# Kernel tuning notes

Hardware: AMD Instinct MI355X
Metric: run time of the kernel (lower is better)

Reference implementation:

```python
import jax, jax.numpy as jnp
import numpy as np

IN_F = 512
OUT_F = 512
ALPHA = 0.2   # LeakyReLU negative slope
NEG_INF = -9e15


def setup_inputs() -> dict:
    key = jax.random.key(0)
    k1, k2, k3, k4 = jax.random.split(key, 4)
    B, S = 8, 2048
    hidden_state = jax.random.normal(k1, (B, S, IN_F), dtype=jnp.float32)
    adjacent_matrix = jax.random.uniform(k2, (B, S, S), dtype=jnp.float32)
    # nn.Linear weight (no bias): stored as [out, in] in torch; we keep [in, out] for x @ W
    bound = 1.0 / np.sqrt(IN_F)
    W = jax.random.uniform(k3, (IN_F, OUT_F), dtype=jnp.float32, minval=-bound, maxval=bound)
    # xavier_uniform with gain=1.414 on a: shape [2*out, 1]
    a_bound = 1.414 * np.sqrt(6.0 / (2 * OUT_F + 1))
    a = jax.random.uniform(k4, (2 * OUT_F, 1), dtype=jnp.float32, minval=-a_bound, maxval=a_bound)
    return {"hidden_state": hidden_state, "adjacent_matrix": adjacent_matrix, "W": W, "a": a}


def reference(hidden_state, adjacent_matrix, W, a):
    # Wh: [B, S, out]
    Wh = jnp.einsum('bsi,io->bso', hidden_state, W)
    # additive attention: Wh1 + Wh2^T -> [B, S, S]
    Wh1 = Wh @ a[:OUT_F, :]            # [B, S, 1]
    Wh2 = Wh @ a[OUT_F:, :]            # [B, S, 1]
    e = Wh1 + jnp.swapaxes(Wh2, 1, 2)  # [B, S, S]
    e = jax.nn.leaky_relu(e, negative_slope=ALPHA)
    attention = jnp.where(adjacent_matrix > 0.5, e, NEG_INF)
    # NOTE: original softmaxes over dim=1 (the *row* index), faithfully reproduced
    attention = jax.nn.softmax(attention, axis=1)
    # dropout is identity at inference (training=False)
    h_prime = jnp.einsum('bst,bto->bso', attention, Wh)
    return jax.nn.elu(h_prime)  # concat=True path
```

## Files before the change

kernel.cpp:

```cpp
#include <hip/hip_runtime.h>
#include <hip/hip_bf16.h>
#include <stdint.h>

#define SDIM 2048
#define BDIM 8
#define FDIM 512
constexpr float ALPHA = 0.2f;

typedef __attribute__((ext_vector_type(8))) short bf16x8;
typedef __attribute__((ext_vector_type(4))) float f32x4;

__device__ __forceinline__ unsigned short f2bf(float x) {
  __hip_bfloat16 h = __float2bfloat16(x);
  return *reinterpret_cast<unsigned short*>(&h);
}

__device__ __forceinline__ void gload_lds16(const void* g, void* l) {
  __builtin_amdgcn_global_load_lds(
      (const __attribute__((address_space(1))) unsigned int*)(uintptr_t)g,
      (__attribute__((address_space(3))) unsigned int*)(uintptr_t)l,
      16, 0, 0);
}

__global__ void k0_prep(const float* __restrict__ W, const float* __restrict__ a,
                        float* __restrict__ wa, __hip_bfloat16* __restrict__ WT) {
  int i = blockIdx.x;
  int lane = threadIdx.x;
  float s1 = 0.f, s2 = 0.f;
  for (int o = lane; o < FDIM; o += 64) {
    float w = W[i * FDIM + o];
    s1 += w * a[o];
    s2 += w * a[FDIM + o];
    WT[o * FDIM + i] = __float2bfloat16(w);
  }
  #pragma unroll
  for (int off = 32; off > 0; off >>= 1) {
    s1 += __shfl_down(s1, off);
    s2 += __shfl_down(s2, off);
  }
  if (lane == 0) { wa[i] = s1; wa[FDIM + i] = s2; }
}

__global__ __launch_bounds__(256) void k1_rows(const float* __restrict__ H,
                                               const float* __restrict__ wa,
                                               float* __restrict__ Wh1, float* __restrict__ Wh2,
                                               __hip_bfloat16* __restrict__ Hb) {
  int wid = threadIdx.x >> 6, lane = threadIdx.x & 63;
  long r = (long)blockIdx.x * 4 + wid;
  const float* hr = H + r * FDIM;
  float4 v0 = ((const float4*)hr)[lane];
  float4 v1 = ((const float4*)hr)[lane + 64];
  float4 wa10 = ((const float4*)wa)[lane];
  float4 wa11 = ((const float4*)wa)[lane + 64];
  float4 wa20 = ((const float4*)(wa + FDIM))[lane];
  float4 wa21 = ((const float4*)(wa + FDIM))[lane + 64];
  float s1 = v0.x*wa10.x + v0.y*wa10.y + v0.z*wa10.z + v0.w*wa10.w
           + v1.x*wa11.x + v1.y*wa11.y + v1.z*wa11.z + v1.w*wa11.w;
  float s2 = v0.x*wa20.x + v0.y*wa20.y + v0.z*wa20.z + v0.w*wa20.w
           + v1.x*wa21.x + v1.y*wa21.y + v1.z*wa21.z + v1.w*wa21.w;
  ushort4 u0 = { f2bf(v0.x), f2bf(v0.y), f2bf(v0.z), f2bf(v0.w) };
  ushort4 u1 = { f2bf(v1.x), f2bf(v1.y), f2bf(v1.z), f2bf(v1.w) };
  ushort4* hb = (ushort4*)(Hb + r * FDIM);
  hb[lane] = u0;
  hb[lane + 64] = u1;
  #pragma unroll
  for (int off = 32; off > 0; off >>= 1) {
    s1 += __shfl_down(s1, off);
    s2 += __shfl_down(s2, off);
  }
  if (lane == 0) { Wh1[r] = s1; Wh2[r] = s2; }
}

__global__ __launch_bounds__(256) void k2_z(const float* __restrict__ adj,
                                            const float* __restrict__ Wh1,
                                            const float* __restrict__ Wh2,
                                            float* __restrict__ Zp) {
  int t = blockIdx.x * 256 + threadIdx.x;
  int b = blockIdx.y;
  int c = blockIdx.z;
  float w2 = Wh2[b * SDIM + t];
  const float* arow = adj + ((long)b * SDIM + c * 64) * SDIM + t;
  const float* w1p = Wh1 + b * SDIM + c * 64;
  float z = 0.f;
  #pragma unroll 8
  for (int s = 0; s < 64; ++s) {
    float av = arow[(long)s * SDIM];
    float e = w1p[s] + w2;
    e = e > 0.f ? e : ALPHA * e;
    float p = __expf(e);
    z += (av > 0.5f) ? p : 0.f;
  }
  Zp[(b * 32 + c) * SDIM + t] = z;
}

__global__ void k2b_rz(const float* __restrict__ Zp, float* __restrict__ rZ) {
  int idx = blockIdx.x * 256 + threadIdx.x;
  int b = idx >> 11, t = idx & 2047;
  float z = 0.f;
  #pragma unroll
  for (int c = 0; c < 32; ++c) z += Zp[(b * 32 + c) * SDIM + t];
  rZ[idx] = 1.0f / z;
}

__global__ __launch_bounds__(256) void k3_gemm(const __hip_bfloat16* __restrict__ WTm,
                                               const __hip_bfloat16* __restrict__ Hb,
                                               const float* __restrict__ rZ,
                                               __hip_bfloat16* __restrict__ VT) {
  __shared__ __align__(16) __hip_bfloat16 Asm[2][128 * 32];
  __shared__ __align__(16) __hip_bfloat16 Bsm[2][128 * 32];
  const int o0 = blockIdx.x * 128;
  const int t0 = blockIdx.y * 128;
  const int b = blockIdx.z;
  const int tid = threadIdx.x;
  const int w = tid >> 6, lane = tid & 63;
  const int wm = w >> 1, wn = w & 1;
  const int fr = lane & 15, fq = lane >> 4;
  const int lr = lane >> 2, lb = (lane & 3) * 16;

  const __hip_bfloat16* Abase = WTm + (long)o0 * FDIM;
  const __hip_bfloat16* Bbase = Hb + ((long)b * SDIM + t0) * FDIM;

  f32x4 acc[4][4] = {};

  auto stage = [&](int kk, int buf) {
    #pragma unroll
    for (int g = 0; g < 2; ++g) {
      int rbase = g * 64 + w * 16;
      int row = rbase + lr;
      gload_lds16((const char*)(Abase + (long)row * FDIM + kk * 32) + lb,
                  (char*)&Asm[buf][0] + rbase * 64);
      gload_lds16((const char*)(Bbase + (long)row * FDIM + kk * 32) + lb,
                  (char*)&Bsm[buf][0] + rbase * 64);
    }
  };

  stage(0, 0);
  __syncthreads();
  for (int kk = 0; kk < 16; ++kk) {
    int cur = kk & 1;
    if (kk < 15) stage(kk + 1, cur ^ 1);
    bf16x8 af[4], bf_[4];
    #pragma unroll
    for (int mf = 0; mf < 4; ++mf)
      af[mf] = *(const bf16x8*)((const char*)&Asm[cur][0] + (wm * 64 + mf * 16 + fr) * 64 + fq * 16);
    #pragma unroll
    for (int nf = 0; nf < 4; ++nf)
      bf_[nf] = *(const bf16x8*)((const char*)&Bsm[cur][0] + (wn * 64 + nf * 16 + fr) * 64 + fq * 16);
    #pragma unroll
    for (int mf = 0; mf < 4; ++mf)
      #pragma unroll
      for (int nf = 0; nf < 4; ++nf)
        acc[mf][nf] = __builtin_amdgcn_mfma_f32_16x16x32_bf16(af[mf], bf_[nf], acc[mf][nf], 0, 0, 0);
    __syncthreads();
  }

  #pragma unroll
  for (int nf = 0; nf < 4; ++nf) {
    int t = t0 + wn * 64 + nf * 16 + fr;
    float rz = rZ[b * SDIM + t];
    #pragma unroll
    for (int mf = 0; mf < 4; ++mf) {
      #pragma unroll
      for (int r = 0; r < 4; ++r) {
        int o = o0 + wm * 64 + mf * 16 + fq * 4 + r;
        VT[((long)(b * FDIM + o)) * SDIM + t] = __float2bfloat16(acc[mf][nf][r] * rz);
      }
    }
  }
}

__global__ __launch_bounds__(256, 2) void k4_pv(const float* __restrict__ adj,
                                                const float* __restrict__ Wh1,
                                                const float* __restrict__ Wh2,
                                                const __hip_bfloat16* __restrict__ VT,
                                                float* __restrict__ out) {
  __shared__ __align__(16) __hip_bfloat16 Vsm[2][256 * 32];
  __shared__ __align__(16) float AdjSm[3][64 * 32];
  __shared__ __align__(16) __hip_bfloat16 Psm[2][64 * 32];
  __shared__ __align__(16) float w2l[SDIM];
  const int b  = blockIdx.x;
  const int s0 = blockIdx.y * 64;
  const int ob = blockIdx.z * 256;
  const int tid = threadIdx.x;
  const int w = tid >> 6, lane = tid & 63;
  const int fr = lane & 15, fq = lane >> 4;

  const int brow = w * 16 + (lane & 15);
  const int bchk = lane >> 4;

  const float w1 = Wh1[b * SDIM + s0 + brow];
  const char* adjG = (const char*)(adj + ((long)b * SDIM + s0) * SDIM);
  const char* vtG  = (const char*)(VT + ((long)(b * FDIM + ob)) * SDIM);
  const char* w2G  = (const char*)(Wh2 + (long)b * SDIM);

  f32x4 acc[4][4] = {};

  auto stageV = [&](int p, int buf) {
    #pragma unroll
    for (int g = 0; g < 4; ++g) {
      int row = w * 64 + g * 16 + (lane & 15);
      gload_lds16(vtG + ((long)row * SDIM + p * 32 + (lane >> 4) * 8) * 2,
                  (char*)&Vsm[buf][0] + w * 4096 + g * 1024);
    }
  };
  auto stageA = [&](int p, int slot) {
    int row = w * 16 + (lane & 15);
    const char* src = adjG + ((long)row * SDIM + p * 32 + (lane >> 4) * 8) * 4;
    gload_lds16(src,      (char*)&AdjSm[slot][0] + w * 2048);
    gload_lds16(src + 16, (char*)&AdjSm[slot][0] + w * 2048 + 1024);
  };
  auto build = [&](int p, int pbuf, int slot) {
    const char* abase = (const char*)&AdjSm[slot][0] + w * 2048 + lane * 16;
    float4 a0 = *(const float4*)(abase);
    float4 a1 = *(const float4*)(abase + 1024);
    const float* wrow = &w2l[p * 32 + bchk * 8];
    float4 q0 = *(const float4*)(wrow);
    float4 q1 = *(const float4*)(wrow + 4);
    float aa[8] = {a0.x,a0.y,a0.z,a0.w,a1.x,a1.y,a1.z,a1.w};
    float qq[8] = {q0.x,q0.y,q0.z,q0.w,q1.x,q1.y,q1.z,q1.w};
    bf16x8 pv;
    #pragma unroll
    for (int i = 0; i < 8; ++i) {
      float e = w1 + qq[i];
      e = fmaxf(e, ALPHA * e);
      float pr = (aa[i] > 0.5f) ? __expf(e) : 0.f;
      pv[i] = (short)f2bf(pr);
    }
    *(bf16x8*)((char*)&Psm[pbuf][0] + w * 1024 + lane * 16) = pv;
  };

  #pragma unroll
  for (int g = 0; g < 2; ++g)
    gload_lds16(w2G + w * 2048 + g * 1024 + lane * 16,
                (char*)w2l + w * 2048 + g * 1024);
  stageA(0, 0);
  stageA(1, 1);
  stageV(0, 0);
  asm volatile("s_waitcnt vmcnt(0)" ::: "memory");
  __syncthreads();
  build(0, 0, 0);
  stageA(2, 2);
  asm volatile("s_waitcnt lgkmcnt(0)" ::: "memory");
  __builtin_amdgcn_sched_barrier(0);
  __builtin_amdgcn_s_barrier();

  int slotS = 0;
  int slotB = 1;
  for (int p = 0; p < 64; ++p) {
    const int cur = p & 1;
    if (p <= 62) stageV(p + 1, cur ^ 1);
    if (p <= 60) stageA(p + 3, slotS);
    __builtin_amdgcn_sched_barrier(0);

    bf16x8 pa[4], vb[4];
    #pragma unroll
    for (int mf = 0; mf < 4; ++mf)
      pa[mf] = *(const bf16x8*)((const char*)&Psm[cur][0] + mf * 1024 + lane * 16);
    #pragma unroll
    for (int nf = 0; nf < 4; ++nf)
      vb[nf] = *(const bf16x8*)((const char*)&Vsm[cur][0] + w * 4096 + nf * 1024 + lane * 16);
    __builtin_amdgcn_s_setprio(1);
    #pragma unroll
    for (int mf = 0; mf < 4; ++mf)
      #pragma unroll
      for (int nf = 0; nf < 4; ++nf)
        acc[mf][nf] = __builtin_amdgcn_mfma_f32_16x16x32_bf16(pa[mf], vb[nf], acc[mf][nf], 0, 0, 0);
    __builtin_amdgcn_s_setprio(0);

    if (p <= 62) build(p + 1, cur ^ 1, slotB);

    if (p <= 60) { asm volatile("s_waitcnt vmcnt(2)" ::: "memory"); }
    else         { asm volatile("s_waitcnt vmcnt(0)" ::: "memory"); }
    asm volatile("s_waitcnt lgkmcnt(0)" ::: "memory");
    __builtin_amdgcn_sched_barrier(0);
    __builtin_amdgcn_s_barrier();

    slotS = slotB;
    slotB = (slotB == 2) ? 0 : slotB + 1;
  }

  float* orow = out + ((long)b * SDIM + s0) * FDIM + ob + w * 64;
  #pragma unroll
  for (int mf = 0; mf < 4; ++mf) {
    #pragma unroll
    for (int nf = 0; nf < 4; ++nf) {
      #pragma unroll
      for (int r = 0; r < 4; ++r) {
        int s = mf * 16 + fq * 4 + r;
        int o = nf * 16 + fr;
        float x = acc[mf][nf][r];
        x = x > 0.f ? x : (__expf(x) - 1.f);
        orow[(long)s * FDIM + o] = x;
      }
    }
  }
}

extern "C" void kernel_launch(void* const* d_in, const int* in_sizes, int n_in,
                              void* d_out, int out_size, void* d_ws, size_t ws_size,
                              hipStream_t stream) {
  const float* H   = (const float*)d_in[0];
  const float* adj = (const float*)d_in[1];
  const float* W   = (const float*)d_in[2];
  const float* a   = (const float*)d_in[3];
  float* out = (float*)d_out;
  char* ws = (char*)d_ws;

  __hip_bfloat16* VT  = (__hip_bfloat16*)(ws + 0);
  __hip_bfloat16* Hb  = (__hip_bfloat16*)(ws + 16777216);
  __hip_bfloat16* WT  = (__hip_bfloat16*)(ws + 33554432);
  float* wa  = (float*)(ws + 34078720);
  float* Wh1 = (float*)(ws + 34082816);
  float* Wh2 = (float*)(ws + 34148352);
  float* rZ  = (float*)(ws + 34213888);
  float* Zp  = (float*)(ws + 34279424);

  hipLaunchKernelGGL(k0_prep, dim3(512), dim3(64), 0, stream, W, a, wa, WT);
  hipLaunchKernelGGL(k1_rows, dim3(4096), dim3(256), 0, stream, H, wa, Wh1, Wh2, Hb);
  hipLaunchKernelGGL(k2_z, dim3(8, 8, 32), dim3(256), 0, stream, adj, Wh1, Wh2, Zp);
  hipLaunchKernelGGL(k2b_rz, dim3(64), dim3(256), 0, stream, Zp, rZ);
  hipLaunchKernelGGL(k3_gemm, dim3(4, 16, 8), dim3(256), 0, stream, WT, Hb, rZ, VT);
  hipLaunchKernelGGL(k4_pv, dim3(8, 32, 2), dim3(256), 0, stream, adj, Wh1, Wh2, VT, out);
}
```

Before: 149.1 us.

## Load V fragments directly from global memory and reorder the P/V pipeline

Drops the LDS double buffer for V and has each lane load its MFMA B-operand fragments straight from global memory into registers every iteration. The adjacency staging is rearranged so each row's 32 floats sit contiguously, and the third adjacency stage is issued in the prologue. The loop now builds the next P tile before the MFMAs, not after, and the explicit vmcnt waits and priority bumps are removed. This saves LDS traffic and LDS capacity for V, but exposes global-load latency inside each iteration and relies on compiler-inserted waits for correct ordering of the async adjacency loads.

```diff
diff --git a/kernel.cpp b/kernel.cpp
--- a/kernel.cpp
+++ b/kernel.cpp
@@ -174,7 +174,6 @@
                                                 const float* __restrict__ Wh2,
                                                 const __hip_bfloat16* __restrict__ VT,
                                                 float* __restrict__ out) {
-  __shared__ __align__(16) __hip_bfloat16 Vsm[2][256 * 32];
   __shared__ __align__(16) float AdjSm[3][64 * 32];
   __shared__ __align__(16) __hip_bfloat16 Psm[2][64 * 32];
   __shared__ __align__(16) float w2l[SDIM];
@@ -185,35 +184,26 @@
   const int w = tid >> 6, lane = tid & 63;
   const int fr = lane & 15, fq = lane >> 4;
 
-  const int brow = w * 16 + (lane & 15);
-  const int bchk = lane >> 4;
-
-  const float w1 = Wh1[b * SDIM + s0 + brow];
+  const float w1 = Wh1[b * SDIM + s0 + w * 16 + fr];
   const char* adjG = (const char*)(adj + ((long)b * SDIM + s0) * SDIM);
-  const char* vtG  = (const char*)(VT + ((long)(b * FDIM + ob)) * SDIM);
   const char* w2G  = (const char*)(Wh2 + (long)b * SDIM);
+  const __hip_bfloat16* vbase = VT + ((long)(b * FDIM + ob + w * 64 + fr)) * SDIM;
 
   f32x4 acc[4][4] = {};
 
-  auto stageV = [&](int p, int buf) {
-    #pragma unroll
-    for (int g = 0; g < 4; ++g) {
-      int row = w * 64 + g * 16 + (lane & 15);
-      gload_lds16(vtG + ((long)row * SDIM + p * 32 + (lane >> 4) * 8) * 2,
-                  (char*)&Vsm[buf][0] + w * 4096 + g * 1024);
-    }
-  };
   auto stageA = [&](int p, int slot) {
-    int row = w * 16 + (lane & 15);
-    const char* src = adjG + ((long)row * SDIM + p * 32 + (lane >> 4) * 8) * 4;
-    gload_lds16(src,      (char*)&AdjSm[slot][0] + w * 2048);
-    gload_lds16(src + 16, (char*)&AdjSm[slot][0] + w * 2048 + 1024);
+    #pragma unroll
+    for (int g = 0; g < 2; ++g) {
+      int row = w * 16 + g * 8 + (lane >> 3);
+      gload_lds16(adjG + ((long)row * SDIM + p * 32 + (lane & 7) * 4) * 4,
+                  (char*)&AdjSm[slot][0] + (w * 16 + g * 8) * 128);
+    }
   };
   auto build = [&](int p, int pbuf, int slot) {
-    const char* abase = (const char*)&AdjSm[slot][0] + w * 2048 + lane * 16;
+    const char* abase = (const char*)&AdjSm[slot][0] + w * 2048 + fr * 128 + fq * 32;
     float4 a0 = *(const float4*)(abase);
-    float4 a1 = *(const float4*)(abase + 1024);
-    const float* wrow = &w2l[p * 32 + bchk * 8];
+    float4 a1 = *(const float4*)(abase + 16);
+    const float* wrow = &w2l[p * 32 + fq * 8];
     float4 q0 = *(const float4*)(wrow);
     float4 q1 = *(const float4*)(wrow + 4);
     float aa[8] = {a0.x,a0.y,a0.z,a0.w,a1.x,a1.y,a1.z,a1.w};
@@ -235,11 +225,10 @@
                 (char*)w2l + w * 2048 + g * 1024);
   stageA(0, 0);
   stageA(1, 1);
-  stageV(0, 0);
+  stageA(2, 2);
   asm volatile("s_waitcnt vmcnt(0)" ::: "memory");
   __syncthreads();
   build(0, 0, 0);
-  stageA(2, 2);
   asm volatile("s_waitcnt lgkmcnt(0)" ::: "memory");
   __builtin_amdgcn_sched_barrier(0);
   __builtin_amdgcn_s_barrier();
@@ -248,29 +237,26 @@
   int slotB = 1;
   for (int p = 0; p < 64; ++p) {
     const int cur = p & 1;
-    if (p <= 62) stageV(p + 1, cur ^ 1);
+    bf16x8 vb[4];
+    #pragma unroll
+    for (int nf = 0; nf < 4; ++nf)
+      vb[nf] = *(const bf16x8*)(vbase + (long)nf * 16 * SDIM + p * 32 + fq * 8);
     if (p <= 60) stageA(p + 3, slotS);
-    __builtin_amdgcn_sched_barrier(0);
-
-    bf16x8 pa[4], vb[4];
+
+    bf16x8 pa[4];
     #pragma unroll
     for (int mf = 0; mf < 4; ++mf)
       pa[mf] = *(const bf16x8*)((const char*)&Psm[cur][0] + mf * 1024 + lane * 16);
-    #pragma unroll
-    for (int nf = 0; nf < 4; ++nf)
-      vb[nf] = *(const bf16x8*)((const char*)&Vsm[cur][0] + w * 4096 + nf * 1024 + lane * 16);
-    __builtin_amdgcn_s_setprio(1);
+
+    if (p <= 62) build(p + 1, cur ^ 1, slotB);
+    __builtin_amdgcn_sched_barrier(0);
+
     #pragma unroll
     for (int mf = 0; mf < 4; ++mf)
       #pragma unroll
       for (int nf = 0; nf < 4; ++nf)
         acc[mf][nf] = __builtin_amdgcn_mfma_f32_16x16x32_bf16(pa[mf], vb[nf], acc[mf][nf], 0, 0, 0);
-    __builtin_amdgcn_s_setprio(0);
-
-    if (p <= 62) build(p + 1, cur ^ 1, slotB);
-
-    if (p <= 60) { asm volatile("s_waitcnt vmcnt(2)" ::: "memory"); }
-    else         { asm volatile("s_waitcnt vmcnt(0)" ::: "memory"); }
+
     asm volatile("s_waitcnt lgkmcnt(0)" ::: "memory");
     __builtin_amdgcn_sched_barrier(0);
     __builtin_amdgcn_s_barrier();
```

Result: no change. 150.3 us (+0.8%).

## Materialize bf16 attention numerators in z pass and stream them into PV GEMM

Applied to the files above, without the earlier changes.

The z-reduction kernel now also writes the masked exp numerators as a bf16 matrix P, so the PV kernel loads P tiles directly instead of re-reading fp32 adjacency and recomputing leaky-relu/exp per output block. This halves the bytes the PV kernel reads per tile and removes its build stage and related LDS buffers, and adds XOR-swizzled LDS layouts for P and V fragments. In exchange, it adds a 64 MB intermediate write plus read, and the pipeline now waits for all loads each iteration.

```diff
diff --git a/kernel.cpp b/kernel.cpp
--- a/kernel.cpp
+++ b/kernel.cpp
@@ -74,21 +74,24 @@
 __global__ __launch_bounds__(256) void k2_z(const float* __restrict__ adj,
                                             const float* __restrict__ Wh1,
                                             const float* __restrict__ Wh2,
-                                            float* __restrict__ Zp) {
+                                            float* __restrict__ Zp,
+                                            __hip_bfloat16* __restrict__ P) {
   int t = blockIdx.x * 256 + threadIdx.x;
   int b = blockIdx.y;
   int c = blockIdx.z;
   float w2 = Wh2[b * SDIM + t];
   const float* arow = adj + ((long)b * SDIM + c * 64) * SDIM + t;
   const float* w1p = Wh1 + b * SDIM + c * 64;
+  __hip_bfloat16* prow = P + ((long)b * SDIM + c * 64) * SDIM + t;
   float z = 0.f;
   #pragma unroll 8
   for (int s = 0; s < 64; ++s) {
     float av = arow[(long)s * SDIM];
     float e = w1p[s] + w2;
-    e = e > 0.f ? e : ALPHA * e;
-    float p = __expf(e);
-    z += (av > 0.5f) ? p : 0.f;
+    e = fmaxf(e, ALPHA * e);
+    float p = (av > 0.5f) ? __expf(e) : 0.f;
+    z += p;
+    prow[(long)s * SDIM] = __float2bfloat16(p);
   }
   Zp[(b * 32 + c) * SDIM + t] = z;
 }
@@ -169,96 +172,59 @@
   }
 }
 
-__global__ __launch_bounds__(256, 2) void k4_pv(const float* __restrict__ adj,
-                                                const float* __restrict__ Wh1,
-                                                const float* __restrict__ Wh2,
+__global__ __launch_bounds__(256, 2) void k4_pv(const __hip_bfloat16* __restrict__ P,
                                                 const __hip_bfloat16* __restrict__ VT,
                                                 float* __restrict__ out) {
   __shared__ __align__(16) __hip_bfloat16 Vsm[2][256 * 32];
-  __shared__ __align__(16) float AdjSm[3][64 * 32];
   __shared__ __align__(16) __hip_bfloat16 Psm[2][64 * 32];
-  __shared__ __align__(16) float w2l[SDIM];
   const int b  = blockIdx.x;
   const int s0 = blockIdx.y * 64;
   const int ob = blockIdx.z * 256;
   const int tid = threadIdx.x;
   const int w = tid >> 6, lane = tid & 63;
   const int fr = lane & 15, fq = lane >> 4;
-
-  const int brow = w * 16 + (lane & 15);
-  const int bchk = lane >> 4;
-
-  const float w1 = Wh1[b * SDIM + s0 + brow];
-  const char* adjG = (const char*)(adj + ((long)b * SDIM + s0) * SDIM);
-  const char* vtG  = (const char*)(VT + ((long)(b * FDIM + ob)) * SDIM);
-  const char* w2G  = (const char*)(Wh2 + (long)b * SDIM);
+  const int srow = lane >> 2;
+  const int sgam = (lane & 3) ^ ((lane >> 2) & 3);
+
+  const char* vtG = (const char*)(VT + ((long)(b * FDIM + ob)) * SDIM);
+  const char* pG  = (const char*)(P + ((long)(b * SDIM + s0)) * SDIM);
 
   f32x4 acc[4][4] = {};
 
   auto stageV = [&](int p, int buf) {
     #pragma unroll
     for (int g = 0; g < 4; ++g) {
-      int row = w * 64 + g * 16 + (lane & 15);
-      gload_lds16(vtG + ((long)row * SDIM + p * 32 + (lane >> 4) * 8) * 2,
+      int row = w * 64 + g * 16 + srow;
+      gload_lds16(vtG + ((long)row * SDIM + p * 32 + sgam * 8) * 2,
                   (char*)&Vsm[buf][0] + w * 4096 + g * 1024);
     }
   };
-  auto stageA = [&](int p, int slot) {
-    int row = w * 16 + (lane & 15);
-    const char* src = adjG + ((long)row * SDIM + p * 32 + (lane >> 4) * 8) * 4;
-    gload_lds16(src,      (char*)&AdjSm[slot][0] + w * 2048);
-    gload_lds16(src + 16, (char*)&AdjSm[slot][0] + w * 2048 + 1024);
+  auto stageP = [&](int p, int buf) {
+    int row = w * 16 + srow;
+    gload_lds16(pG + ((long)row * SDIM + p * 32 + sgam * 8) * 2,
+                (char*)&Psm[buf][0] + w * 1024);
   };
-  auto build = [&](int p, int pbuf, int slot) {
-    const char* abase = (const char*)&AdjSm[slot][0] + w * 2048 + lane * 16;
-    float4 a0 = *(const float4*)(abase);
-    float4 a1 = *(const float4*)(abase + 1024);
-    const float* wrow = &w2l[p * 32 + bchk * 8];
-    float4 q0 = *(const float4*)(wrow);
-    float4 q1 = *(const float4*)(wrow + 4);
-    float aa[8] = {a0.x,a0.y,a0.z,a0.w,a1.x,a1.y,a1.z,a1.w};
-    float qq[8] = {q0.x,q0.y,q0.z,q0.w,q1.x,q1.y,q1.z,q1.w};
-    bf16x8 pv;
-    #pragma unroll
-    for (int i = 0; i < 8; ++i) {
-      float e = w1 + qq[i];
-      e = fmaxf(e, ALPHA * e);
-      float pr = (aa[i] > 0.5f) ? __expf(e) : 0.f;
-      pv[i] = (short)f2bf(pr);
-    }
-    *(bf16x8*)((char*)&Psm[pbuf][0] + w * 1024 + lane * 16) = pv;
-  };
-
-  #pragma unroll
-  for (int g = 0; g < 2; ++g)
-    gload_lds16(w2G + w * 2048 + g * 1024 + lane * 16,
-                (char*)w2l + w * 2048 + g * 1024);
-  stageA(0, 0);
-  stageA(1, 1);
+
   stageV(0, 0);
+  stageP(0, 0);
   asm volatile("s_waitcnt vmcnt(0)" ::: "memory");
-  __syncthreads();
-  build(0, 0, 0);
-  stageA(2, 2);
-  asm volatile("s_waitcnt lgkmcnt(0)" ::: "memory");
   __builtin_amdgcn_sched_barrier(0);
   __builtin_amdgcn_s_barrier();
 
-  int slotS = 0;
-  int slotB = 1;
   for (int p = 0; p < 64; ++p) {
     const int cur = p & 1;
-    if (p <= 62) stageV(p + 1, cur ^ 1);
-    if (p <= 60) stageA(p + 3, slotS);
+    if (p < 63) { stageV(p + 1, cur ^ 1); stageP(p + 1, cur ^ 1); }
     __builtin_amdgcn_sched_barrier(0);
 
     bf16x8 pa[4], vb[4];
     #pragma unroll
     for (int mf = 0; mf < 4; ++mf)
-      pa[mf] = *(const bf16x8*)((const char*)&Psm[cur][0] + mf * 1024 + lane * 16);
+      pa[mf] = *(const bf16x8*)((const char*)&Psm[cur][0] + mf * 1024
+                                + fr * 64 + (fq ^ (fr & 3)) * 16);
     #pragma unroll
     for (int nf = 0; nf < 4; ++nf)
-      vb[nf] = *(const bf16x8*)((const char*)&Vsm[cur][0] + w * 4096 + nf * 1024 + lane * 16);
+      vb[nf] = *(const bf16x8*)((const char*)&Vsm[cur][0] + w * 4096 + nf * 1024
+                                + fr * 64 + (fq ^ (fr & 3)) * 16);
     __builtin_amdgcn_s_setprio(1);
     #pragma unroll
     for (int mf = 0; mf < 4; ++mf)
@@ -267,16 +233,9 @@
         acc[mf][nf] = __builtin_amdgcn_mfma_f32_16x16x32_bf16(pa[mf], vb[nf], acc[mf][nf], 0, 0, 0);
     __builtin_amdgcn_s_setprio(0);
 
-    if (p <= 62) build(p + 1, cur ^ 1, slotB);
-
-    if (p <= 60) { asm volatile("s_waitcnt vmcnt(2)" ::: "memory"); }
-    else         { asm volatile("s_waitcnt vmcnt(0)" ::: "memory"); }
-    asm volatile("s_waitcnt lgkmcnt(0)" ::: "memory");
+    asm volatile("s_waitcnt vmcnt(0) lgkmcnt(0)" ::: "memory");
     __builtin_amdgcn_sched_barrier(0);
     __builtin_amdgcn_s_barrier();
-
-    slotS = slotB;
-    slotB = (slotB == 2) ? 0 : slotB + 1;
   }
 
   float* orow = out + ((long)b * SDIM + s0) * FDIM + ob + w * 64;
@@ -314,11 +273,12 @@
   float* Wh2 = (float*)(ws + 34148352);
   float* rZ  = (float*)(ws + 34213888);
   float* Zp  = (float*)(ws + 34279424);
+  __hip_bfloat16* P = (__hip_bfloat16*)(ws + 37748736);
 
   hipLaunchKernelGGL(k0_prep, dim3(512), dim3(64), 0, stream, W, a, wa, WT);
   hipLaunchKernelGGL(k1_rows, dim3(4096), dim3(256), 0, stream, H, wa, Wh1, Wh2, Hb);
-  hipLaunchKernelGGL(k2_z, dim3(8, 8, 32), dim3(256), 0, stream, adj, Wh1, Wh2, Zp);
+  hipLaunchKernelGGL(k2_z, dim3(8, 8, 32), dim3(256), 0, stream, adj, Wh1, Wh2, Zp, P);
   hipLaunchKernelGGL(k2b_rz, dim3(64), dim3(256), 0, stream, Zp, rZ);
   hipLaunchKernelGGL(k3_gemm, dim3(4, 16, 8), dim3(256), 0, stream, WT, Hb, rZ, VT);
-  hipLaunchKernelGGL(k4_pv, dim3(8, 32, 2), dim3(256), 0, stream, adj, Wh1, Wh2, VT, out);
-}
+  hipLaunchKernelGGL(k4_pv, dim3(8, 32, 2), dim3(256), 0, stream, P, VT, out);
+}
```

Result: faster. 125.0 us (-16.2%).
